# Optimization experiments

Measured on AMD Instinct MI355X. Metric: run time of the kernel, lower is better.

Reference implementation:

```python
import jax, jax.numpy as jnp
import numpy as np

WH, WW = 8, 8
N = WH * WW          # 64 tokens per window
C = 128              # channels
H = 4                # heads
HD = C // H          # head dim = 32
B = 4096             # batch * num_windows
NW = 1024            # windows per image (mask groups)
EPS = 1e-5


def _relative_position_index():
    ch = np.arange(WH)
    cw = np.arange(WW)
    coords = np.stack(np.meshgrid(ch, cw, indexing='ij'))        # (2, WH, WW)
    cf = coords.reshape(2, -1)                                    # (2, N)
    rel = cf[:, :, None] - cf[:, None, :]                         # (2, N, N)
    rel = rel.transpose(1, 2, 0).copy()                           # (N, N, 2)
    rel[:, :, 0] += WH - 1
    rel[:, :, 1] += WW - 1
    rel[:, :, 0] *= 2 * WW - 1
    return rel.sum(-1).astype(np.int32)                           # (N, N)


def setup_inputs() -> dict:
    key = jax.random.key(0)
    ks = jax.random.split(key, 12)
    s = 0.02
    tbl_size = (2 * WH - 1) * (2 * WW - 1)
    return {
        'x': jax.random.normal(ks[0], (B, N, C), jnp.float32),
        'y': jax.random.normal(ks[1], (B, N, C), jnp.float32),
        'mask': jnp.zeros((NW, N, N), jnp.float32),
        'wqkv1': jax.random.normal(ks[2], (C, 3 * C), jnp.float32) * s,
        'bqkv1': jnp.zeros((3 * C,), jnp.float32),
        'wqkv2': jax.random.normal(ks[3], (C, 3 * C), jnp.float32) * s,
        'bqkv2': jnp.zeros((3 * C,), jnp.float32),
        'tbl1': jax.random.normal(ks[4], (tbl_size, H), jnp.float32) * s,
        'tbl2': jax.random.normal(ks[5], (tbl_size, H), jnp.float32) * s,
        'wproj1': jax.random.normal(ks[6], (C, C), jnp.float32) * s,
        'bproj1': jnp.zeros((C,), jnp.float32),
        'wproj2': jax.random.normal(ks[7], (C, C), jnp.float32) * s,
        'bproj2': jnp.zeros((C,), jnp.float32),
        'g1': jnp.ones((C,), jnp.float32),
        'be1': jnp.zeros((C,), jnp.float32),
        'g2': jnp.ones((C,), jnp.float32),
        'be2': jnp.zeros((C,), jnp.float32),
        'rpi': jnp.asarray(_relative_position_index()),
    }


def _layernorm(x, g, b):
    mu = jnp.mean(x, -1, keepdims=True)
    var = jnp.mean(jnp.square(x - mu), -1, keepdims=True)
    return (x - mu) * jax.lax.rsqrt(var + EPS) * g + b


def _qkv(t, w, b):
    q, k, v = jnp.split((t @ w + b).reshape(B, N, 3, H, HD).transpose(2, 0, 3, 1, 4), 3, axis=0)
    return q[0], k[0], v[0]


def reference(x, y, mask, wqkv1, bqkv1, wqkv2, bqkv2, tbl1, tbl2,
              wproj1, bproj1, wproj2, bproj2, g1, be1, g2, be2, rpi):
    q1, k1, v1 = _qkv(x, wqkv1, bqkv1)
    q2, k2, v2 = _qkv(y, wqkv2, bqkv2)
    scale = 1.0 / jnp.sqrt(jnp.float32(C))

    bias1 = tbl1[rpi].transpose(2, 0, 1)   # (H, N, N) gathered from small table
    bias2 = tbl2[rpi].transpose(2, 0, 1)

    attn1 = jnp.einsum('bhnd,bhmd->bhnm', q1, k2) * scale + bias1[None]
    attn2 = jnp.einsum('bhnd,bhmd->bhnm', q2, k1) * scale + bias2[None]

    nW = mask.shape[0]
    attn1 = (attn1.reshape(B // nW, nW, H, N, N) + mask[None, :, None]).reshape(B, H, N, N)
    attn2 = (attn2.reshape(B // nW, nW, H, N, N) + mask[None, :, None]).reshape(B, H, N, N)

    attn1 = jax.nn.softmax(attn1, axis=-1)
    attn2 = jax.nn.softmax(attn2, axis=-1)

    out1 = jnp.einsum('bhnm,bhmd->bhnd', attn1, v2).transpose(0, 2, 1, 3).reshape(B, N, C)
    out2 = jnp.einsum('bhnm,bhmd->bhnd', attn2, v1).transpose(0, 2, 1, 3).reshape(B, N, C)

    out1 = _layernorm(out1 @ wproj1 + bproj1 + x, g1, be1)
    out2 = _layernorm(out2 @ wproj2 + bproj2 + y, g2, be2)
    return out1, out2
```

## Files before the change

### kernel.cpp

```cpp
#include <hip/hip_runtime.h>
#include <stdint.h>


typedef __attribute__((ext_vector_type(8))) short short8;
typedef __attribute__((ext_vector_type(4))) float f32x4;

#define MFMA(a, b, c) __builtin_amdgcn_mfma_f32_16x16x32_bf16((a), (b), (c), 0, 0, 0)

static __device__ __forceinline__ unsigned short f2bf(float f) {
  union { float f; uint32_t u; } v; v.f = f;
  uint32_t u = v.u + (0x7fffu + ((v.u >> 16) & 1u));
  return (unsigned short)(u >> 16);
}

__global__ __launch_bounds__(256) void prep_kernel(
    const float* __restrict__ wqkv1, const float* __restrict__ wqkv2,
    const float* __restrict__ wproj1, const float* __restrict__ wproj2,
    const float* __restrict__ tbl1, const float* __restrict__ tbl2,
    const int* __restrict__ rpi,
    unsigned short* __restrict__ wq1p, unsigned short* __restrict__ wq2p,
    unsigned short* __restrict__ wp1p, unsigned short* __restrict__ wp2p,
    float* __restrict__ bias1, float* __restrict__ bias2) {
  int tid = blockIdx.x * 256 + threadIdx.x;
  if (tid < 12288) {
    const float* W = (tid < 6144) ? wqkv1 : wqkv2;
    unsigned short* P = (tid < 6144) ? wq1p : wq2p;
    int local = (tid < 6144) ? tid : tid - 6144;
    int tile = local >> 6, lane = local & 63;
    int nt = tile >> 2, kt = tile & 3;
    int n = nt * 16 + (lane & 15);
    int kb = kt * 32 + (lane >> 4) * 8;
    unsigned short* dst = P + (size_t)(tile * 64 + lane) * 8;
#pragma unroll
    for (int j = 0; j < 8; ++j) dst[j] = f2bf(W[(kb + j) * 384 + n]);
  } else if (tid < 16384) {
    int local = tid - 12288;
    const float* W = (local < 2048) ? wproj1 : wproj2;
    unsigned short* P = (local < 2048) ? wp1p : wp2p;
    local &= 2047;
    int tile = local >> 6, lane = local & 63;
    int nt = tile >> 2, kt = tile & 3;
    int n = nt * 16 + (lane & 15);
    int kb = kt * 32 + (lane >> 4) * 8;
    unsigned short* dst = P + (size_t)(tile * 64 + lane) * 8;
#pragma unroll
    for (int j = 0; j < 8; ++j) dst[j] = f2bf(W[(kb + j) * 128 + n]);
  } else if (tid < 49152) {
    int local = tid - 16384;
    const float* T = (local < 16384) ? tbl1 : tbl2;
    float* D = (local < 16384) ? bias1 : bias2;
    local &= 16383;
    int h = local >> 12, ij = local & 4095;
    D[local] = T[rpi[ij] * 4 + h];
  }
}

__global__ __launch_bounds__(512, 2) void wca_kernel(
    const float* __restrict__ x, const float* __restrict__ y,
    const float* __restrict__ mask,
    const float* __restrict__ bqkv1, const float* __restrict__ bqkv2,
    const float* __restrict__ bproj1, const float* __restrict__ bproj2,
    const float* __restrict__ g1, const float* __restrict__ be1,
    const float* __restrict__ g2, const float* __restrict__ be2,
    const unsigned short* __restrict__ wq1p, const unsigned short* __restrict__ wq2p,
    const unsigned short* __restrict__ wp1p, const unsigned short* __restrict__ wp2p,
    const float* __restrict__ biasT1, const float* __restrict__ biasT2,
    float* __restrict__ out) {
  __shared__ __align__(16) unsigned short sQ[2][4][64][40];
  __shared__ __align__(16) unsigned short sK[2][4][64][40];
  __shared__ __align__(16) unsigned short sVT[2][4][32][72];
  __shared__ __align__(16) unsigned short sP[4][64][72];

  const int b = blockIdx.x;
  const int tid = (int)threadIdx.x;
  const int wave = tid >> 6;
  const int lane = tid & 63;
  const int quad = lane >> 4;
  const int col = lane & 15;

  {
    const int side = wave >> 2;
    const int ntg = wave & 3;
    const float* src = (side ? y : x) + (size_t)b * 8192;
    const unsigned short* wp = side ? wq2p : wq1p;
    const float* bq = side ? bqkv2 : bqkv1;

    short8 afrag[4][4];
#pragma unroll
    for (int mt = 0; mt < 4; ++mt) {
      int m = mt * 16 + col;
#pragma unroll
      for (int ks = 0; ks < 4; ++ks) {
        const float* p = src + m * 128 + ks * 32 + quad * 8;
        float4 lo = *(const float4*)(p);
        float4 hi = *(const float4*)(p + 4);
        short8 f;
        f[0] = (short)f2bf(lo.x); f[1] = (short)f2bf(lo.y);
        f[2] = (short)f2bf(lo.z); f[3] = (short)f2bf(lo.w);
        f[4] = (short)f2bf(hi.x); f[5] = (short)f2bf(hi.y);
        f[6] = (short)f2bf(hi.z); f[7] = (short)f2bf(hi.w);
        afrag[mt][ks] = f;
      }
    }

#pragma unroll 1
    for (int t = 0; t < 6; ++t) {
      int nt = ntg * 6 + t;
      float bias = bq[nt * 16 + col];
      short8 bfrag[4];
#pragma unroll
      for (int ks = 0; ks < 4; ++ks)
        bfrag[ks] = *(const short8*)(wp + (size_t)((nt * 4 + ks) * 64 + lane) * 8);
      int sel = nt >> 3;
      int cw = (nt & 7) * 16 + col;
      int h = cw >> 5, d = cw & 31;
#pragma unroll
      for (int mt = 0; mt < 4; ++mt) {
        f32x4 acc = {bias, bias, bias, bias};
#pragma unroll
        for (int ks = 0; ks < 4; ++ks) acc = MFMA(afrag[mt][ks], bfrag[ks], acc);
#pragma unroll
        for (int r = 0; r < 4; ++r) {
          int row = mt * 16 + quad * 4 + r;
          unsigned short v = f2bf(acc[r]);
          if (sel == 0)      sQ[side][h][row][d] = v;
          else if (sel == 1) sK[side][h][row][d] = v;
          else               sVT[side][h][d][row] = v;
        }
      }
    }
  }
  __syncthreads();

  {
    const float scale = 0.08838834764831845f;
    const int h = wave & 3;
    const int rh = wave >> 2;
    const float* mbase = mask + (size_t)(b & 1023) * 4096;

#pragma unroll 1
    for (int s = 0; s < 2; ++s) {
      const float* bt = (s == 0 ? biasT1 : biasT2) + h * 4096;

      float bm[2][4][4];
#pragma unroll
      for (int mi = 0; mi < 2; ++mi) {
        int ib = (2 * rh + mi) * 16 + quad * 4;
#pragma unroll
        for (int nt = 0; nt < 4; ++nt) {
          int jj = nt * 16 + col;
#pragma unroll
          for (int r = 0; r < 4; ++r)
            bm[mi][nt][r] = bt[(ib + r) * 64 + jj] + mbase[(ib + r) * 64 + jj];
        }
      }

      short8 qf[2], kf[4];
#pragma unroll
      for (int mi = 0; mi < 2; ++mi)
        qf[mi] = *(const short8*)&sQ[s][h][(2 * rh + mi) * 16 + col][quad * 8];
#pragma unroll
      for (int nt = 0; nt < 4; ++nt)
        kf[nt] = *(const short8*)&sK[1 - s][h][nt * 16 + col][quad * 8];

      float pv[2][4][4];
#pragma unroll
      for (int mi = 0; mi < 2; ++mi)
#pragma unroll
        for (int nt = 0; nt < 4; ++nt) {
          f32x4 acc = {0.f, 0.f, 0.f, 0.f};
          acc = MFMA(qf[mi], kf[nt], acc);
#pragma unroll
          for (int r = 0; r < 4; ++r)
            pv[mi][nt][r] = fmaf(acc[r], scale, bm[mi][nt][r]);
        }

#pragma unroll
      for (int mi = 0; mi < 2; ++mi)
#pragma unroll
        for (int r = 0; r < 4; ++r) {
          float mx = fmaxf(fmaxf(pv[mi][0][r], pv[mi][1][r]),
                           fmaxf(pv[mi][2][r], pv[mi][3][r]));
          mx = fmaxf(mx, __shfl_xor(mx, 1, 16));
          mx = fmaxf(mx, __shfl_xor(mx, 2, 16));
          mx = fmaxf(mx, __shfl_xor(mx, 4, 16));
          mx = fmaxf(mx, __shfl_xor(mx, 8, 16));
          float sum = 0.f;
#pragma unroll
          for (int nt = 0; nt < 4; ++nt) {
            pv[mi][nt][r] = __expf(pv[mi][nt][r] - mx);
            sum += pv[mi][nt][r];
          }
          sum += __shfl_xor(sum, 1, 16);
          sum += __shfl_xor(sum, 2, 16);
          sum += __shfl_xor(sum, 4, 16);
          sum += __shfl_xor(sum, 8, 16);
          float inv = 1.0f / sum;
          int row = (2 * rh + mi) * 16 + quad * 4 + r;
#pragma unroll
          for (int nt = 0; nt < 4; ++nt)
            sP[h][row][nt * 16 + col] = f2bf(pv[mi][nt][r] * inv);
        }

      __syncthreads();

      short8 pf[2][2], vf[2][2];
#pragma unroll
      for (int mi = 0; mi < 2; ++mi)
#pragma unroll
        for (int ks = 0; ks < 2; ++ks)
          pf[mi][ks] = *(const short8*)&sP[h][(2 * rh + mi) * 16 + col][ks * 32 + quad * 8];
#pragma unroll
      for (int dt = 0; dt < 2; ++dt)
#pragma unroll
        for (int ks = 0; ks < 2; ++ks)
          vf[dt][ks] = *(const short8*)&sVT[1 - s][h][dt * 16 + col][ks * 32 + quad * 8];

      unsigned short* sO = &sQ[s][0][0][0];
#pragma unroll
      for (int mi = 0; mi < 2; ++mi)
#pragma unroll
        for (int dt = 0; dt < 2; ++dt) {
          f32x4 acc = {0.f, 0.f, 0.f, 0.f};
#pragma unroll
          for (int ks = 0; ks < 2; ++ks) acc = MFMA(pf[mi][ks], vf[dt][ks], acc);
#pragma unroll
          for (int r = 0; r < 4; ++r) {
            int row = (2 * rh + mi) * 16 + quad * 4 + r;
            sO[row * 136 + h * 32 + dt * 16 + col] = f2bf(acc[r]);
          }
        }
      __syncthreads();
    }
  }

  {
    const int side = wave >> 2;
    const int mt = wave & 3;
    const unsigned short* sO = &sQ[side][0][0][0];
    const unsigned short* wpp = side ? wp2p : wp1p;
    const float* bp = side ? bproj2 : bproj1;
    const float* gg = side ? g2 : g1;
    const float* bb = side ? be2 : be1;
    const float* res = (side ? y : x) + (size_t)b * 8192;
    float* o = out + (size_t)side * 33554432 + (size_t)b * 8192;

    short8 af[4];
#pragma unroll
    for (int ks = 0; ks < 4; ++ks)
      af[ks] = *(const short8*)&sO[(mt * 16 + col) * 136 + ks * 32 + quad * 8];

    float vals[8][4];
#pragma unroll
    for (int nt = 0; nt < 8; ++nt) {
      float bias = bp[nt * 16 + col];
      f32x4 acc = {bias, bias, bias, bias};
#pragma unroll
      for (int ks = 0; ks < 4; ++ks)
        acc = MFMA(af[ks], *(const short8*)(wpp + (size_t)((nt * 4 + ks) * 64 + lane) * 8), acc);
#pragma unroll
      for (int r = 0; r < 4; ++r)
        vals[nt][r] = acc[r] + res[(mt * 16 + quad * 4 + r) * 128 + nt * 16 + col];
    }

#pragma unroll
    for (int r = 0; r < 4; ++r) {
      float sum = 0.f;
#pragma unroll
      for (int nt = 0; nt < 8; ++nt) sum += vals[nt][r];
      sum += __shfl_xor(sum, 1, 16);
      sum += __shfl_xor(sum, 2, 16);
      sum += __shfl_xor(sum, 4, 16);
      sum += __shfl_xor(sum, 8, 16);
      float mean = sum * 0.0078125f;
      float vsum = 0.f;
#pragma unroll
      for (int nt = 0; nt < 8; ++nt) {
        float d = vals[nt][r] - mean;
        vsum += d * d;
      }
      vsum += __shfl_xor(vsum, 1, 16);
      vsum += __shfl_xor(vsum, 2, 16);
      vsum += __shfl_xor(vsum, 4, 16);
      vsum += __shfl_xor(vsum, 8, 16);
      float rstd = rsqrtf(vsum * 0.0078125f + 1e-5f);
      int row = mt * 16 + quad * 4 + r;
#pragma unroll
      for (int nt = 0; nt < 8; ++nt) {
        int c = nt * 16 + col;
        o[row * 128 + c] = (vals[nt][r] - mean) * rstd * gg[c] + bb[c];
      }
    }
  }
}

extern "C" void kernel_launch(void* const* d_in, const int* in_sizes, int n_in,
                              void* d_out, int out_size, void* d_ws, size_t ws_size,
                              hipStream_t stream) {
  const float* x = (const float*)d_in[0];
  const float* y = (const float*)d_in[1];
  const float* mask = (const float*)d_in[2];
  const float* wqkv1 = (const float*)d_in[3];
  const float* bqkv1 = (const float*)d_in[4];
  const float* wqkv2 = (const float*)d_in[5];
  const float* bqkv2 = (const float*)d_in[6];
  const float* tbl1 = (const float*)d_in[7];
  const float* tbl2 = (const float*)d_in[8];
  const float* wproj1 = (const float*)d_in[9];
  const float* bproj1 = (const float*)d_in[10];
  const float* wproj2 = (const float*)d_in[11];
  const float* bproj2 = (const float*)d_in[12];
  const float* g1 = (const float*)d_in[13];
  const float* be1 = (const float*)d_in[14];
  const float* g2 = (const float*)d_in[15];
  const float* be2 = (const float*)d_in[16];
  const int* rpi = (const int*)d_in[17];

  char* ws = (char*)d_ws;
  unsigned short* wq1p = (unsigned short*)(ws + 0);
  unsigned short* wq2p = (unsigned short*)(ws + 98304);
  unsigned short* wp1p = (unsigned short*)(ws + 196608);
  unsigned short* wp2p = (unsigned short*)(ws + 229376);
  float* bias1 = (float*)(ws + 262144);
  float* bias2 = (float*)(ws + 327680);

  prep_kernel<<<dim3(192), dim3(256), 0, stream>>>(
      wqkv1, wqkv2, wproj1, wproj2, tbl1, tbl2, rpi,
      wq1p, wq2p, wp1p, wp2p, bias1, bias2);

  wca_kernel<<<dim3(4096), dim3(512), 0, stream>>>(
      x, y, mask, bqkv1, bqkv2, bproj1, bproj2,
      g1, be1, g2, be2, wq1p, wq2p, wp1p, wp2p, bias1, bias2,
      (float*)d_out);
}
```

Baseline: 797.9 us.

## Keep attention probabilities and V in registers to cut LDS and raise occupancy

Computes scores as K·Q transposed so each lane holds a full column of softmax inputs. P is then redistributed to MFMA A-operand layout with cross-lane shuffles instead of an LDS round trip. V projections stay packed in registers and are written into the freed K buffer only when needed, which removes the sP and sVT shared arrays. The smaller LDS footprint lets launch bounds ask for 4 blocks per CU. Bias tables are pre-permuted into fragment order so each lane does vectorized loads. This adds many shuffles and extra barriers, and the higher occupancy target squeezes the register budget, which may cause spills.

Measured after the change: 879.8 us. +10.3%, slower.

```diff
diff --git a/kernel.cpp b/kernel.cpp
--- a/kernel.cpp
+++ b/kernel.cpp
@@ -3,7 +3,9 @@
 
 
 typedef __attribute__((ext_vector_type(8))) short short8;
+typedef __attribute__((ext_vector_type(4))) short short4v;
 typedef __attribute__((ext_vector_type(4))) float f32x4;
+typedef __attribute__((ext_vector_type(2))) unsigned int uint2v;
 
 #define MFMA(a, b, c) __builtin_amdgcn_mfma_f32_16x16x32_bf16((a), (b), (c), 0, 0, 0)
 
@@ -11,6 +13,9 @@
   union { float f; uint32_t u; } v; v.f = f;
   uint32_t u = v.u + (0x7fffu + ((v.u >> 16) & 1u));
   return (unsigned short)(u >> 16);
+}
+static __device__ __forceinline__ uint32_t pk2(float a, float b) {
+  return (uint32_t)f2bf(a) | ((uint32_t)f2bf(b) << 16);
 }
 
 __global__ __launch_bounds__(256) void prep_kernel(
@@ -50,12 +55,18 @@
     const float* T = (local < 16384) ? tbl1 : tbl2;
     float* D = (local < 16384) ? bias1 : bias2;
     local &= 16383;
-    int h = local >> 12, ij = local & 4095;
-    D[local] = T[rpi[ij] * 4 + h];
+    int r = local & 3;
+    int ln = (local >> 2) & 63;
+    int mt = (local >> 8) & 3;
+    int ni = (local >> 10) & 3;
+    int h = local >> 12;
+    int i = ni * 16 + (ln & 15);
+    int j = mt * 16 + (ln >> 4) * 4 + r;
+    D[local] = T[rpi[i * 64 + j] * 4 + h];
   }
 }
 
-__global__ __launch_bounds__(512, 2) void wca_kernel(
+__global__ __launch_bounds__(512, 4) void wca_kernel(
     const float* __restrict__ x, const float* __restrict__ y,
     const float* __restrict__ mask,
     const float* __restrict__ bqkv1, const float* __restrict__ bqkv2,
@@ -66,10 +77,8 @@
     const unsigned short* __restrict__ wp1p, const unsigned short* __restrict__ wp2p,
     const float* __restrict__ biasT1, const float* __restrict__ biasT2,
     float* __restrict__ out) {
-  __shared__ __align__(16) unsigned short sQ[2][4][64][40];
+  __shared__ __align__(16) unsigned short sQ[2][4][64][36];
   __shared__ __align__(16) unsigned short sK[2][4][64][40];
-  __shared__ __align__(16) unsigned short sVT[2][4][32][72];
-  __shared__ __align__(16) unsigned short sP[4][64][72];
 
   const int b = blockIdx.x;
   const int tid = (int)threadIdx.x;
@@ -77,13 +86,15 @@
   const int lane = tid & 63;
   const int quad = lane >> 4;
   const int col = lane & 15;
+  const int sideA = wave >> 2;
+  const int ntg = wave & 3;
+
+  uint32_t vpk[2][4][2];
 
   {
-    const int side = wave >> 2;
-    const int ntg = wave & 3;
-    const float* src = (side ? y : x) + (size_t)b * 8192;
-    const unsigned short* wp = side ? wq2p : wq1p;
-    const float* bq = side ? bqkv2 : bqkv1;
+    const float* src = (sideA ? y : x) + (size_t)b * 8192;
+    const unsigned short* wp = sideA ? wq2p : wq1p;
+    const float* bq = sideA ? bqkv2 : bqkv1;
 
     short8 afrag[4][4];
 #pragma unroll
@@ -93,27 +104,26 @@
       for (int ks = 0; ks < 4; ++ks) {
         const float* p = src + m * 128 + ks * 32 + quad * 8;
         float4 lo = *(const float4*)(p);
-        float4 hi = *(const float4*)(p + 4);
+        float4 hi4 = *(const float4*)(p + 4);
         short8 f;
         f[0] = (short)f2bf(lo.x); f[1] = (short)f2bf(lo.y);
         f[2] = (short)f2bf(lo.z); f[3] = (short)f2bf(lo.w);
-        f[4] = (short)f2bf(hi.x); f[5] = (short)f2bf(hi.y);
-        f[6] = (short)f2bf(hi.z); f[7] = (short)f2bf(hi.w);
+        f[4] = (short)f2bf(hi4.x); f[5] = (short)f2bf(hi4.y);
+        f[6] = (short)f2bf(hi4.z); f[7] = (short)f2bf(hi4.w);
         afrag[mt][ks] = f;
       }
     }
 
 #pragma unroll 1
-    for (int t = 0; t < 6; ++t) {
-      int nt = ntg * 6 + t;
+    for (int t = 0; t < 4; ++t) {
+      int nt = ntg + t * 4;
       float bias = bq[nt * 16 + col];
       short8 bfrag[4];
 #pragma unroll
       for (int ks = 0; ks < 4; ++ks)
         bfrag[ks] = *(const short8*)(wp + (size_t)((nt * 4 + ks) * 64 + lane) * 8);
-      int sel = nt >> 3;
       int cw = (nt & 7) * 16 + col;
-      int h = cw >> 5, d = cw & 31;
+      int hq = cw >> 5, d = cw & 31;
 #pragma unroll
       for (int mt = 0; mt < 4; ++mt) {
         f32x4 acc = {bias, bias, bias, bias};
@@ -123,116 +133,167 @@
         for (int r = 0; r < 4; ++r) {
           int row = mt * 16 + quad * 4 + r;
           unsigned short v = f2bf(acc[r]);
-          if (sel == 0)      sQ[side][h][row][d] = v;
-          else if (sel == 1) sK[side][h][row][d] = v;
-          else               sVT[side][h][d][row] = v;
+          if (t < 2) sQ[sideA][hq][row][d] = v;
+          else       sK[sideA][hq][row][d] = v;
         }
+      }
+    }
+
+#pragma unroll
+    for (int vt = 0; vt < 2; ++vt) {
+      int nt = ntg + 16 + vt * 4;
+      float bias = bq[nt * 16 + col];
+      short8 bfrag[4];
+#pragma unroll
+      for (int ks = 0; ks < 4; ++ks)
+        bfrag[ks] = *(const short8*)(wp + (size_t)((nt * 4 + ks) * 64 + lane) * 8);
+#pragma unroll
+      for (int mt = 0; mt < 4; ++mt) {
+        f32x4 acc = {bias, bias, bias, bias};
+#pragma unroll
+        for (int ks = 0; ks < 4; ++ks) acc = MFMA(afrag[mt][ks], bfrag[ks], acc);
+        vpk[vt][mt][0] = pk2(acc[0], acc[1]);
+        vpk[vt][mt][1] = pk2(acc[2], acc[3]);
       }
     }
   }
   __syncthreads();
 
-  {
+#pragma unroll 1
+  for (int s = 0; s < 2; ++s) {
     const float scale = 0.08838834764831845f;
     const int h = wave & 3;
-    const int rh = wave >> 2;
+    const int qh = wave >> 2;
     const float* mbase = mask + (size_t)(b & 1023) * 4096;
-
-#pragma unroll 1
-    for (int s = 0; s < 2; ++s) {
-      const float* bt = (s == 0 ? biasT1 : biasT2) + h * 4096;
-
-      float bm[2][4][4];
-#pragma unroll
-      for (int mi = 0; mi < 2; ++mi) {
-        int ib = (2 * rh + mi) * 16 + quad * 4;
-#pragma unroll
-        for (int nt = 0; nt < 4; ++nt) {
-          int jj = nt * 16 + col;
-#pragma unroll
-          for (int r = 0; r < 4; ++r)
-            bm[mi][nt][r] = bt[(ib + r) * 64 + jj] + mbase[(ib + r) * 64 + jj];
+    const float* bL = (s == 0 ? biasT1 : biasT2) + h * 4096;
+    const int g0 = ((2 * quad) & 3) * 16 + col;
+    const int g1 = ((2 * quad + 1) & 3) * 16 + col;
+    const int hi = quad >> 1;
+
+    short8 kf[4];
+#pragma unroll
+    for (int mt = 0; mt < 4; ++mt)
+      kf[mt] = *(const short8*)&sK[1 - s][h][mt * 16 + col][quad * 8];
+    short8 qf[2];
+#pragma unroll
+    for (int ni = 0; ni < 2; ++ni) {
+      const short4v* qp = (const short4v*)&sQ[s][h][(qh * 2 + ni) * 16 + col][0];
+      short4v qa = qp[2 * quad], qb = qp[2 * quad + 1];
+      qf[ni] = __builtin_shufflevector(qa, qb, 0, 1, 2, 3, 4, 5, 6, 7);
+    }
+
+    float bm[2][4][4];
+#pragma unroll
+    for (int ni = 0; ni < 2; ++ni)
+#pragma unroll
+      for (int mt = 0; mt < 4; ++mt) {
+        f32x4 bb = *(const f32x4*)(bL + (size_t)(((qh * 2 + ni) * 4 + mt) * 64 + lane) * 4);
+        f32x4 mm = *(const f32x4*)(mbase + ((qh * 2 + ni) * 16 + col) * 64 + mt * 16 + quad * 4);
+#pragma unroll
+        for (int r = 0; r < 4; ++r) bm[ni][mt][r] = bb[r] + mm[r];
+      }
+
+    float sv[2][4][4];
+#pragma unroll
+    for (int ni = 0; ni < 2; ++ni)
+#pragma unroll
+      for (int mt = 0; mt < 4; ++mt) {
+        f32x4 acc = {0.f, 0.f, 0.f, 0.f};
+        acc = MFMA(kf[mt], qf[ni], acc);
+#pragma unroll
+        for (int r = 0; r < 4; ++r) sv[ni][mt][r] = fmaf(acc[r], scale, bm[ni][mt][r]);
+      }
+
+    __syncthreads();
+    if (sideA == 1 - s) {
+      unsigned short* vbw = &sK[1 - s][0][0][0];
+#pragma unroll
+      for (int vt = 0; vt < 2; ++vt) {
+        int nt = ntg + 16 + vt * 4;
+        int cw = (nt & 7) * 16 + col;
+        int hv = cw >> 5, dv = cw & 31;
+#pragma unroll
+        for (int mt = 0; mt < 4; ++mt) {
+          uint2v vv; vv.x = vpk[vt][mt][0]; vv.y = vpk[vt][mt][1];
+          *(uint2v*)(vbw + hv * 2304 + dv * 72 + mt * 16 + quad * 4) = vv;
         }
       }
-
-      short8 qf[2], kf[4];
-#pragma unroll
-      for (int mi = 0; mi < 2; ++mi)
-        qf[mi] = *(const short8*)&sQ[s][h][(2 * rh + mi) * 16 + col][quad * 8];
-#pragma unroll
-      for (int nt = 0; nt < 4; ++nt)
-        kf[nt] = *(const short8*)&sK[1 - s][h][nt * 16 + col][quad * 8];
-
-      float pv[2][4][4];
-#pragma unroll
-      for (int mi = 0; mi < 2; ++mi)
-#pragma unroll
-        for (int nt = 0; nt < 4; ++nt) {
-          f32x4 acc = {0.f, 0.f, 0.f, 0.f};
-          acc = MFMA(qf[mi], kf[nt], acc);
-#pragma unroll
-          for (int r = 0; r < 4; ++r)
-            pv[mi][nt][r] = fmaf(acc[r], scale, bm[mi][nt][r]);
+    }
+    __syncthreads();
+
+    const unsigned short* vb = &sK[1 - s][0][0][0];
+    short8 vf[2][2];
+#pragma unroll
+    for (int dt = 0; dt < 2; ++dt)
+#pragma unroll
+      for (int ks = 0; ks < 2; ++ks)
+        vf[dt][ks] = *(const short8*)(vb + h * 2304 + (dt * 16 + col) * 72 + ks * 32 + quad * 8);
+
+    uint32_t pk[2][4][2];
+#pragma unroll
+    for (int ni = 0; ni < 2; ++ni) {
+      float mx = sv[ni][0][0];
+#pragma unroll
+      for (int mt = 0; mt < 4; ++mt)
+#pragma unroll
+        for (int r = 0; r < 4; ++r) mx = fmaxf(mx, sv[ni][mt][r]);
+      mx = fmaxf(mx, __shfl_xor(mx, 16));
+      mx = fmaxf(mx, __shfl_xor(mx, 32));
+      float sum = 0.f;
+#pragma unroll
+      for (int mt = 0; mt < 4; ++mt)
+#pragma unroll
+        for (int r = 0; r < 4; ++r) {
+          float e = __expf(sv[ni][mt][r] - mx);
+          sv[ni][mt][r] = e;
+          sum += e;
         }
-
-#pragma unroll
-      for (int mi = 0; mi < 2; ++mi)
-#pragma unroll
-        for (int r = 0; r < 4; ++r) {
-          float mx = fmaxf(fmaxf(pv[mi][0][r], pv[mi][1][r]),
-                           fmaxf(pv[mi][2][r], pv[mi][3][r]));
-          mx = fmaxf(mx, __shfl_xor(mx, 1, 16));
-          mx = fmaxf(mx, __shfl_xor(mx, 2, 16));
-          mx = fmaxf(mx, __shfl_xor(mx, 4, 16));
-          mx = fmaxf(mx, __shfl_xor(mx, 8, 16));
-          float sum = 0.f;
-#pragma unroll
-          for (int nt = 0; nt < 4; ++nt) {
-            pv[mi][nt][r] = __expf(pv[mi][nt][r] - mx);
-            sum += pv[mi][nt][r];
-          }
-          sum += __shfl_xor(sum, 1, 16);
-          sum += __shfl_xor(sum, 2, 16);
-          sum += __shfl_xor(sum, 4, 16);
-          sum += __shfl_xor(sum, 8, 16);
-          float inv = 1.0f / sum;
-          int row = (2 * rh + mi) * 16 + quad * 4 + r;
-#pragma unroll
-          for (int nt = 0; nt < 4; ++nt)
-            sP[h][row][nt * 16 + col] = f2bf(pv[mi][nt][r] * inv);
-        }
-
-      __syncthreads();
-
-      short8 pf[2][2], vf[2][2];
-#pragma unroll
-      for (int mi = 0; mi < 2; ++mi)
-#pragma unroll
-        for (int ks = 0; ks < 2; ++ks)
-          pf[mi][ks] = *(const short8*)&sP[h][(2 * rh + mi) * 16 + col][ks * 32 + quad * 8];
-#pragma unroll
-      for (int dt = 0; dt < 2; ++dt)
-#pragma unroll
-        for (int ks = 0; ks < 2; ++ks)
-          vf[dt][ks] = *(const short8*)&sVT[1 - s][h][dt * 16 + col][ks * 32 + quad * 8];
-
-      unsigned short* sO = &sQ[s][0][0][0];
-#pragma unroll
-      for (int mi = 0; mi < 2; ++mi)
-#pragma unroll
-        for (int dt = 0; dt < 2; ++dt) {
-          f32x4 acc = {0.f, 0.f, 0.f, 0.f};
-#pragma unroll
-          for (int ks = 0; ks < 2; ++ks) acc = MFMA(pf[mi][ks], vf[dt][ks], acc);
-#pragma unroll
-          for (int r = 0; r < 4; ++r) {
-            int row = (2 * rh + mi) * 16 + quad * 4 + r;
-            sO[row * 136 + h * 32 + dt * 16 + col] = f2bf(acc[r]);
-          }
-        }
-      __syncthreads();
-    }
+      sum += __shfl_xor(sum, 16);
+      sum += __shfl_xor(sum, 32);
+      float inv = 1.0f / sum;
+#pragma unroll
+      for (int mt = 0; mt < 4; ++mt) {
+        pk[ni][mt][0] = pk2(sv[ni][mt][0] * inv, sv[ni][mt][1] * inv);
+        pk[ni][mt][1] = pk2(sv[ni][mt][2] * inv, sv[ni][mt][3] * inv);
+      }
+    }
+
+    short8 af[2][2];
+#pragma unroll
+    for (int ni = 0; ni < 2; ++ni)
+#pragma unroll
+      for (int ks = 0; ks < 2; ++ks) {
+        union { uint32_t u[4]; short8 v8; } w;
+        uint32_t alo, ahi;
+        alo = (uint32_t)__shfl((int)pk[ni][2 * ks][0], g0);
+        ahi = (uint32_t)__shfl((int)pk[ni][2 * ks + 1][0], g0);
+        w.u[0] = hi ? ahi : alo;
+        alo = (uint32_t)__shfl((int)pk[ni][2 * ks][1], g0);
+        ahi = (uint32_t)__shfl((int)pk[ni][2 * ks + 1][1], g0);
+        w.u[1] = hi ? ahi : alo;
+        alo = (uint32_t)__shfl((int)pk[ni][2 * ks][0], g1);
+        ahi = (uint32_t)__shfl((int)pk[ni][2 * ks + 1][0], g1);
+        w.u[2] = hi ? ahi : alo;
+        alo = (uint32_t)__shfl((int)pk[ni][2 * ks][1], g1);
+        ahi = (uint32_t)__shfl((int)pk[ni][2 * ks + 1][1], g1);
+        w.u[3] = hi ? ahi : alo;
+        af[ni][ks] = w.v8;
+      }
+
+    unsigned short* ob = &sQ[s][0][0][0];
+#pragma unroll
+    for (int ni = 0; ni < 2; ++ni)
+#pragma unroll
+      for (int dt = 0; dt < 2; ++dt) {
+        f32x4 o = {0.f, 0.f, 0.f, 0.f};
+        o = MFMA(af[ni][0], vf[dt][0], o);
+        o = MFMA(af[ni][1], vf[dt][1], o);
+#pragma unroll
+        for (int r = 0; r < 4; ++r)
+          ob[((qh * 2 + ni) * 16 + quad * 4 + r) * 136 + h * 32 + dt * 16 + col] = f2bf(o[r]);
+      }
   }
+  __syncthreads();
 
   {
     const int side = wave >> 2;
@@ -276,8 +337,8 @@
       float vsum = 0.f;
 #pragma unroll
       for (int nt = 0; nt < 8; ++nt) {
-        float d = vals[nt][r] - mean;
-        vsum += d * d;
+        float dd = vals[nt][r] - mean;
+        vsum += dd * dd;
       }
       vsum += __shfl_xor(vsum, 1, 16);
       vsum += __shfl_xor(vsum, 2, 16);
```
